# Optimization experiments

Measured on AMD Instinct MI355X. Metric: run time of the kernel, lower is better.

The kernel has to match this reference:

```python
import jax, jax.numpy as jnp
import numpy as np
from jax import lax


def _ln(x, gamma, beta, eps=1e-5):
    m = jnp.mean(x, -1, keepdims=True)
    v = jnp.mean(jnp.square(x - m), -1, keepdims=True)
    return (x - m) * lax.rsqrt(v + eps) * gamma + beta


def setup_inputs() -> dict:
    key = jax.random.key(0)
    ks = jax.random.split(key, 12)
    B, C, L = 16, 22, 3000
    D, D2, E, T, K = 64, 256, 8, 4, 13
    s = 0.02
    f32 = jnp.float32
    return dict(
        x_stream=jax.random.normal(ks[0], (B, C, L), f32),
        task_ids=jax.random.randint(ks[1], (B,), 0, T),
        conv_w=jax.random.normal(ks[2], (D, C, K), f32) * s,
        conv_b=jnp.zeros((D,), f32),
        cls_token=jax.random.normal(ks[3], (1, 1, D), f32) * s,
        tok_g=jnp.ones((D,), f32), tok_b=jnp.zeros((D,), f32),
        ds_conv_w=jax.random.normal(ks[4], (D2, 1, 1, K), f32) * s,
        ds_conv_b=jnp.zeros((D2,), f32),
        ds_comp_w=jax.random.normal(ks[5], (D2, D2, D), f32) * s,
        ds_comp_b=jnp.zeros((D2,), f32),
        ds_g=jnp.ones((D2,), f32), ds_b=jnp.zeros((D2,), f32),
        task_embed=jax.random.normal(ks[6], (T, D2), f32) * s,
        gate_w=jax.random.normal(ks[7], (2 * D2, E), f32) * s,
        gate_b=jnp.zeros((E,), f32),
        exp_w=jax.random.normal(ks[8], (E, D2, D2), f32) * s,
        exp_b=jnp.zeros((E, D2), f32),
        uni_w=jax.random.normal(ks[9], (D2, D2), f32) * s,
        uni_b=jnp.zeros((D2,), f32),
        out_g=jnp.ones((D2,), f32), out_b=jnp.zeros((D2,), f32),
    )


def reference(x_stream, task_ids, conv_w, conv_b, cls_token, tok_g, tok_b,
              ds_conv_w, ds_conv_b, ds_comp_w, ds_comp_b, ds_g, ds_b,
              task_embed, gate_w, gate_b, exp_w, exp_b, uni_w, uni_b,
              out_g, out_b):
    gelu = lambda x: jax.nn.gelu(x, approximate=False)
    # --- Tokenize1D: conv1d(stride 2, pad 6) -> GELU -> maxpool(3,3) -> cls cat -> LN
    h = lax.conv_general_dilated(x_stream, conv_w, (2,), [(6, 6)],
                                 dimension_numbers=('NCH', 'OIH', 'NCH')) + conv_b[:, None]
    h = gelu(h)
    h = lax.reduce_window(h, -jnp.inf, lax.max, (1, 1, 3), (1, 1, 3), 'VALID')
    h = jnp.transpose(h, (0, 2, 1))                       # [B, N0, D]
    B = h.shape[0]
    cls = jnp.broadcast_to(cls_token, (B, 1, cls_token.shape[-1]))
    h = jnp.concatenate([cls, h], axis=1)                 # [B, N, D]
    h = _ln(h, tok_g, tok_b)
    # --- DSConvBlock (depth 1): conv2d 1->D2 over (1,13), compress over dim, LN, GELU
    z = jnp.transpose(h, (0, 2, 1))[:, None]              # [B, 1, D, N]
    z = lax.conv_general_dilated(z, ds_conv_w, (1, 1), [(0, 0), (6, 6)],
                                 dimension_numbers=('NCHW', 'OIHW', 'NCHW'))
    z = z + ds_conv_b[:, None, None]                      # [B, D2, D, N]
    z = jnp.einsum('bcdn,ocd->bno', z, ds_comp_w) + ds_comp_b  # compress -> [B, N, D2]
    tokens = gelu(_ln(z, ds_g, ds_b))
    # --- TaskAwareMoE (eval: no dropout, no noise)
    Bn, N, D2 = tokens.shape
    t_vec = task_embed[task_ids]                          # [B, D2]
    T_cat = jnp.concatenate([tokens, jnp.broadcast_to(t_vec[:, None], (Bn, N, D2))], -1)
    logits = T_cat @ gate_w + gate_b                      # [B, N, E]
    topk_vals, topk_idx = lax.top_k(logits, 2)
    gates_k = jax.nn.softmax(topk_vals, axis=-1)          # softmax over top-k (rest are -inf -> 0)
    bi = jnp.arange(Bn)[:, None, None]
    ni = jnp.arange(N)[None, :, None]
    gates = jnp.zeros_like(logits).at[bi, ni, topk_idx].set(gates_k)
    expert_outs = gelu(jnp.einsum('bnd,edf->bnef', tokens, exp_w) + exp_b)  # [B,N,E,D2]
    T_task = jnp.einsum('bne,bnef->bnf', gates, expert_outs)
    T_univ = gelu(tokens @ uni_w + uni_b)
    omega = 1.0 - jnp.max(gates, axis=-1, keepdims=True)
    out = _ln(T_task + omega * T_univ, out_g, out_b)
    return out[:, 0, :]
```

## Files before the change

### kernel.cpp

```cpp
#include <hip/hip_runtime.h>
#include <hip/hip_bf16.h>
#include <math.h>

__device__ __forceinline__ float us2f(unsigned short u) {
    union { unsigned int i; float f; } cv;
    cv.i = ((unsigned int)u) << 16;
    return cv.f;
}

__device__ __forceinline__ int detect_bf(const void* ones_vec) {
    return ((const unsigned int*)ones_vec)[0] == 0x3F803F80u;
}

template<int BF>
__device__ __forceinline__ float ldg(const void* p, int i) {
    return BF ? us2f(((const unsigned short*)p)[i]) : ((const float*)p)[i];
}

__device__ __forceinline__ float wave_sum64(float v) {
#pragma unroll
    for (int m = 32; m > 0; m >>= 1) v += __shfl_xor(v, m, 64);
    return v;
}

__device__ __forceinline__ float gelu_exact(float x) {
    return 0.5f * x * (1.0f + erff(x * 0.7071067811865475f));
}

__device__ __forceinline__ float bsum16(float v, float* sh16) {
    int lane = threadIdx.x & 63, w = threadIdx.x >> 6;
    v = wave_sum64(v);
    __syncthreads();
    if (lane == 0) sh16[w] = v;
    __syncthreads();
    float s = 0;
#pragma unroll
    for (int i = 0; i < 16; ++i) s += sh16[i];
    return s;
}

#define SMEM1_BYTES 41216

template<int BF>
__device__ void stage1_m2(char* smem,
    const void* __restrict__ comp_w, const void* __restrict__ dconv_w,
    const void* __restrict__ dconv_b, const void* __restrict__ comp_b,
    float* __restrict__ M2, float* __restrict__ BE)
{
    int t = threadIdx.x, w = t >> 6, lane = t & 63;
    float* s_dsw = (float*)smem;
    float* s_dcb = s_dsw + 1792;
    float* sred  = s_dcb + 256;
    for (int i = t; i < 1792; i += 512) {
        int c = i / 7, j = i - c * 7;
        s_dsw[i] = ldg<BF>(dconv_w, c * 13 + 6 + j);
    }
    for (int i = t; i < 256; i += 512) s_dcb[i] = ldg<BF>(dconv_b, i);
    __syncthreads();

    int o = blockIdx.x;
    float a0 = 0, a1 = 0, a2 = 0, a3 = 0, a4 = 0, a5 = 0, a6 = 0, ab = 0;
    int base = o * 16384 + lane;
    int c0 = w * 32;
#pragma unroll 8
    for (int ci = 0; ci < 32; ++ci) {
        int c = c0 + ci;
        float wv = ldg<BF>(comp_w, base + c * 64);
        const float* ds = &s_dsw[c * 7];
        a0 += wv * ds[0]; a1 += wv * ds[1]; a2 += wv * ds[2]; a3 += wv * ds[3];
        a4 += wv * ds[4]; a5 += wv * ds[5]; a6 += wv * ds[6];
        ab += wv * s_dcb[c];
    }
    sred[(w * 8 + 0) * 64 + lane] = a0;
    sred[(w * 8 + 1) * 64 + lane] = a1;
    sred[(w * 8 + 2) * 64 + lane] = a2;
    sred[(w * 8 + 3) * 64 + lane] = a3;
    sred[(w * 8 + 4) * 64 + lane] = a4;
    sred[(w * 8 + 5) * 64 + lane] = a5;
    sred[(w * 8 + 6) * 64 + lane] = a6;
    sred[(w * 8 + 7) * 64 + lane] = ab;
    __syncthreads();
    if (t < 448) {
        int j = t >> 6, d = t & 63;
        float s = 0;
#pragma unroll
        for (int ww = 0; ww < 8; ++ww) s += sred[(ww * 8 + j) * 64 + d];
        M2[(j * 64 + d) * 256 + o] = s;
    } else {
        float s = 0;
#pragma unroll
        for (int ww = 0; ww < 8; ++ww) s += sred[(ww * 8 + 7) * 64 + lane];
        s = wave_sum64(s);
        if (lane == 0) BE[o] = ldg<BF>(comp_b, o) + s;
    }
}

template<int BF>
__device__ void stage1_tok(char* smem,
    const void* __restrict__ x, const void* __restrict__ conv_w,
    const void* __restrict__ conv_b, const void* __restrict__ cls,
    const void* __restrict__ tok_g, const void* __restrict__ tok_b,
    float* __restrict__ H)
{
    int t = threadIdx.x, b = blockIdx.x - 256;
    float* sx = (float*)smem;
    for (int i = t; i < 902; i += 512) {
        int c = i / 41, p = i - c * 41;
        sx[i] = ldg<BF>(x, (b * 22 + c) * 3000 + p);
    }
    int w = t >> 6, lane = t & 63, tt = w - 1;
    float val = 0.0f;
    if (BF) {
        unsigned short* swt = (unsigned short*)(smem + 3616);
        const unsigned short* cwu = (const unsigned short*)conv_w;
        for (int i = t; i < 64 * 286; i += 512) {
            int d = i / 286, r = i - d * 286;
            swt[r * 64 + d] = cwu[i];
        }
        __syncthreads();
        if (w == 0) val = ldg<BF>(cls, lane);
        else if (w <= 6) {
            float cb = ldg<BF>(conv_b, lane);
            float p0 = cb, p1 = cb, p2 = cb;
            for (int c = 0; c < 22; ++c) {
                const float* xr = &sx[c * 41];
#pragma unroll
                for (int k = 0; k < 13; ++k) {
                    float wv = us2f(swt[(c * 13 + k) * 64 + lane]);
                    int i0 = 6 * tt - 6 + k;
                    if (i0 >= 0)     p0 += xr[i0] * wv;
                    if (i0 + 2 >= 0) p1 += xr[i0 + 2] * wv;
                    if (i0 + 4 >= 0) p2 += xr[i0 + 4] * wv;
                }
            }
            val = fmaxf(fmaxf(gelu_exact(p0), gelu_exact(p1)), gelu_exact(p2));
        }
    } else {
        float* schunk = (float*)(smem + 3616);
        float cb = ldg<BF>(conv_b, lane);
        float p0 = cb, p1 = cb, p2 = cb;
        for (int c0 = 0; c0 < 22; c0 += 8) {
            int csz = (22 - c0 < 8) ? (22 - c0) : 8;
            int n = csz * 13 * 64;
            __syncthreads();
            for (int i = t; i < n; i += 512) {
                int d = i / (csz * 13), r = i - d * (csz * 13);
                schunk[r * 64 + d] = ldg<BF>(conv_w, d * 286 + c0 * 13 + r);
            }
            __syncthreads();
            if (w >= 1 && w <= 6) {
                for (int cc = 0; cc < csz; ++cc) {
                    const float* xr = &sx[(c0 + cc) * 41];
#pragma unroll
                    for (int k = 0; k < 13; ++k) {
                        float wv = schunk[(cc * 13 + k) * 64 + lane];
                        int i0 = 6 * tt - 6 + k;
                        if (i0 >= 0)     p0 += xr[i0] * wv;
                        if (i0 + 2 >= 0) p1 += xr[i0 + 2] * wv;
                        if (i0 + 4 >= 0) p2 += xr[i0 + 4] * wv;
                    }
                }
            }
        }
        val = (w == 0) ? ldg<BF>(cls, lane)
                       : fmaxf(fmaxf(gelu_exact(p0), gelu_exact(p1)), gelu_exact(p2));
    }
    if (w <= 6) {
        float mean = wave_sum64(val) * (1.0f / 64.0f);
        float dv = val - mean;
        float var = wave_sum64(dv * dv) * (1.0f / 64.0f);
        float hn = dv * rsqrtf(var + 1e-5f) * ldg<BF>(tok_g, lane) + ldg<BF>(tok_b, lane);
        H[b * 448 + w * 64 + lane] = hn;
    }
}

__global__ __launch_bounds__(512) void k_stage1(
    const void* __restrict__ x, const void* __restrict__ conv_w,
    const void* __restrict__ conv_b, const void* __restrict__ cls,
    const void* __restrict__ tok_g, const void* __restrict__ tok_b,
    const void* __restrict__ comp_w, const void* __restrict__ dconv_w,
    const void* __restrict__ dconv_b, const void* __restrict__ comp_b,
    float* __restrict__ H, float* __restrict__ M2, float* __restrict__ BE)
{
    __shared__ char smem[SMEM1_BYTES];
    int bf = detect_bf(tok_g);
    if (blockIdx.x < 256) {
        if (bf) stage1_m2<1>(smem, comp_w, dconv_w, dconv_b, comp_b, M2, BE);
        else    stage1_m2<0>(smem, comp_w, dconv_w, dconv_b, comp_b, M2, BE);
    } else {
        if (bf) stage1_tok<1>(smem, x, conv_w, conv_b, cls, tok_g, tok_b, H);
        else    stage1_tok<0>(smem, x, conv_w, conv_b, cls, tok_g, tok_b, H);
    }
}

template<int BF>
__device__ void stage2_body(char* smem,
    const float* __restrict__ H, const float* __restrict__ M2,
    const float* __restrict__ BE, const int* __restrict__ task_ids,
    const void* __restrict__ ds_g, const void* __restrict__ ds_b,
    const void* __restrict__ task_embed,
    const void* __restrict__ gate_w, const void* __restrict__ gate_b,
    const void* __restrict__ exp_w, const void* __restrict__ exp_b,
    const void* __restrict__ uni_w, const void* __restrict__ uni_b,
    const void* __restrict__ out_g, const void* __restrict__ out_b,
    void* __restrict__ out)
{
    float* sh_h   = (float*)smem;
    float* shp0   = sh_h + 448;
    float* shp1   = shp0 + 1024;
    float* shp2   = shp1 + 1024;
    float* sh_tok = shp2 + 1024;
    float* sh16   = sh_tok + 256;
    float* sh_g32 = sh16 + 16;
    float* sh_sc  = sh_g32 + 32;
    int*   sh_e   = (int*)(sh_sc + 4);

    int t = threadIdx.x, b = blockIdx.x;
    int o = t & 255, q = t >> 8, lane = t & 63, w = t >> 6;

    for (int i = t; i < 448; i += 1024) sh_h[i] = H[b * 448 + i];
    __syncthreads();

    float p = 0;
    int jd0 = q * 112;
#pragma unroll 8
    for (int j = 0; j < 112; ++j) {
        int jd = jd0 + j;
        p += M2[jd * 256 + o] * sh_h[jd];
    }
    shp0[q * 256 + o] = p;
    __syncthreads();

    float z = 0, dz = 0, tok = 0;
    if (t < 256)
        z = BE[o] + ((shp0[o] + shp0[256 + o]) + (shp0[512 + o] + shp0[768 + o]));
    float mean = bsum16((t < 256) ? z : 0.0f, sh16) * (1.0f / 256.0f);
    dz = z - mean;
    float var = bsum16((t < 256) ? dz * dz : 0.0f, sh16) * (1.0f / 256.0f);
    if (t < 256) {
        tok = gelu_exact(dz * rsqrtf(var + 1e-5f) * ldg<BF>(ds_g, o) + ldg<BF>(ds_b, o));
        sh_tok[o] = tok;
    }
    __syncthreads();

    int task = task_ids[b];
    {
        float tko = sh_tok[o];
        float tvo = ldg<BF>(task_embed, task * 256 + o);
        int ea = q * 2, eb = q * 2 + 1;
        float p0 = tko * ldg<BF>(gate_w, o * 8 + ea) + tvo * ldg<BF>(gate_w, (256 + o) * 8 + ea);
        float p1 = tko * ldg<BF>(gate_w, o * 8 + eb) + tvo * ldg<BF>(gate_w, (256 + o) * 8 + eb);
        p0 = wave_sum64(p0);
        p1 = wave_sum64(p1);
        if (lane == 0) { sh_g32[w * 2] = p0; sh_g32[w * 2 + 1] = p1; }
    }
    __syncthreads();
    if (t == 0) {
        float lg[8];
#pragma unroll
        for (int e = 0; e < 8; ++e) {
            int qq = e >> 1, r = e & 1;
            float s = ldg<BF>(gate_b, e);
#pragma unroll
            for (int i = 0; i < 4; ++i) s += sh_g32[(qq * 4 + i) * 2 + r];
            lg[e] = s;
        }
        int e0 = 0;
        for (int e = 1; e < 8; ++e) if (lg[e] > lg[e0]) e0 = e;
        int e1 = (e0 == 0) ? 1 : 0;
        for (int e = 0; e < 8; ++e) if (e != e0 && lg[e] > lg[e1]) e1 = e;
        float g0 = 1.0f / (1.0f + expf(lg[e1] - lg[e0]));
        sh_sc[0] = g0; sh_sc[1] = 1.0f - g0; sh_sc[2] = 1.0f - g0;
        sh_e[0] = e0; sh_e[1] = e1;
    }
    __syncthreads();
    int e0 = sh_e[0], e1 = sh_e[1];
    float g0 = sh_sc[0], g1 = sh_sc[1], om = sh_sc[2];

    float a0 = 0, a1 = 0, au = 0;
    int d0 = q * 64;
    int b0 = e0 * 65536 + o, b1 = e1 * 65536 + o;
#pragma unroll 8
    for (int i = 0; i < 64; ++i) {
        int d = d0 + i;
        float tk = sh_tok[d];
        a0 += tk * ldg<BF>(exp_w, b0 + d * 256);
        a1 += tk * ldg<BF>(exp_w, b1 + d * 256);
        au += tk * ldg<BF>(uni_w, o + d * 256);
    }
    shp0[q * 256 + o] = a0;
    shp1[q * 256 + o] = a1;
    shp2[q * 256 + o] = au;
    __syncthreads();

    float y = 0;
    if (t < 256) {
        float s0 = ldg<BF>(exp_b, e0 * 256 + o) + ((shp0[o] + shp0[256 + o]) + (shp0[512 + o] + shp0[768 + o]));
        float s1 = ldg<BF>(exp_b, e1 * 256 + o) + ((shp1[o] + shp1[256 + o]) + (shp1[512 + o] + shp1[768 + o]));
        float su = ldg<BF>(uni_b, o)            + ((shp2[o] + shp2[256 + o]) + (shp2[512 + o] + shp2[768 + o]));
        y = g0 * gelu_exact(s0) + g1 * gelu_exact(s1) + om * gelu_exact(su);
    }
    float m2v = bsum16((t < 256) ? y : 0.0f, sh16) * (1.0f / 256.0f);
    float dy = y - m2v;
    float v2 = bsum16((t < 256) ? dy * dy : 0.0f, sh16) * (1.0f / 256.0f);
    if (t < 256) {
        float res = dy * rsqrtf(v2 + 1e-5f) * ldg<BF>(out_g, o) + ldg<BF>(out_b, o);
        if (BF) ((__hip_bfloat16*)out)[b * 256 + o] = __float2bfloat16(res);
        else    ((float*)out)[b * 256 + o] = res;
    }
}

__global__ __launch_bounds__(1024) void k_stage2(
    const float* __restrict__ H, const float* __restrict__ M2,
    const float* __restrict__ BE, const int* __restrict__ task_ids,
    const void* __restrict__ tok_g,
    const void* __restrict__ ds_g, const void* __restrict__ ds_b,
    const void* __restrict__ task_embed,
    const void* __restrict__ gate_w, const void* __restrict__ gate_b,
    const void* __restrict__ exp_w, const void* __restrict__ exp_b,
    const void* __restrict__ uni_w, const void* __restrict__ uni_b,
    const void* __restrict__ out_g, const void* __restrict__ out_b,
    void* __restrict__ out)
{
    __shared__ char smem[(448 + 3 * 1024 + 256 + 16 + 32 + 4 + 2) * 4 + 16];
    int bf = detect_bf(tok_g);
    if (bf) stage2_body<1>(smem, H, M2, BE, task_ids, ds_g, ds_b, task_embed,
                           gate_w, gate_b, exp_w, exp_b, uni_w, uni_b,
                           out_g, out_b, out);
    else    stage2_body<0>(smem, H, M2, BE, task_ids, ds_g, ds_b, task_embed,
                           gate_w, gate_b, exp_w, exp_b, uni_w, uni_b,
                           out_g, out_b, out);
}

extern "C" void kernel_launch(void* const* d_in, const int* in_sizes, int n_in,
                              void* d_out, int out_size, void* d_ws, size_t ws_size,
                              hipStream_t stream) {
    const void* x         = d_in[0];
    const int* task_ids   = (const int*)d_in[1];
    const void* conv_w    = d_in[2];
    const void* conv_b    = d_in[3];
    const void* cls       = d_in[4];
    const void* tok_g     = d_in[5];
    const void* tok_b     = d_in[6];
    const void* ds_conv_w = d_in[7];
    const void* ds_conv_b = d_in[8];
    const void* ds_comp_w = d_in[9];
    const void* ds_comp_b = d_in[10];
    const void* ds_g      = d_in[11];
    const void* ds_b      = d_in[12];
    const void* task_embed= d_in[13];
    const void* gate_w    = d_in[14];
    const void* gate_b    = d_in[15];
    const void* exp_w     = d_in[16];
    const void* exp_b     = d_in[17];
    const void* uni_w     = d_in[18];
    const void* uni_b     = d_in[19];
    const void* out_g     = d_in[20];
    const void* out_b     = d_in[21];

    float* ws = (float*)d_ws;
    float* H  = ws;
    float* M2 = ws + 7168;
    float* BE = ws + 7168 + 114688;

    hipLaunchKernelGGL(k_stage1, dim3(272), dim3(512), 0, stream,
                       x, conv_w, conv_b, cls, tok_g, tok_b,
                       ds_comp_w, ds_conv_w, ds_conv_b, ds_comp_b,
                       H, M2, BE);
    hipLaunchKernelGGL(k_stage2, dim3(16), dim3(1024), 0, stream,
                       H, M2, BE, task_ids, tok_g, ds_g, ds_b, task_embed,
                       gate_w, gate_b, exp_w, exp_b, uni_w, uni_b,
                       out_g, out_b, d_out);
}
```

Measured before the change: 165.7 us.

## Halve M2 blocks, pad conv input and pre-transpose conv weights into shared memory

The stage-1 grid drops from 272 to 144 blocks: each M2 block now computes two output channels, and the tokenizer blocks start at index 128. The tokenizer zero-pads the input window in shared memory so the boundary branches go away. It stages all conv weights transposed with padding of 65 (bf16 weights packed in pairs), and loads x into registers with float2 reads. Several loops are unrolled 16 instead of 8. Shared memory per block grows to 80000 bytes, which may limit occupancy and add transpose cost.

```diff
diff --git a/kernel.cpp b/kernel.cpp
--- a/kernel.cpp
+++ b/kernel.cpp
@@ -39,7 +39,7 @@
     return s;
 }
 
-#define SMEM1_BYTES 41216
+#define SMEM1_BYTES 80000
 
 template<int BF>
 __device__ void stage1_m2(char* smem,
@@ -58,40 +58,43 @@
     for (int i = t; i < 256; i += 512) s_dcb[i] = ldg<BF>(dconv_b, i);
     __syncthreads();
 
-    int o = blockIdx.x;
-    float a0 = 0, a1 = 0, a2 = 0, a3 = 0, a4 = 0, a5 = 0, a6 = 0, ab = 0;
-    int base = o * 16384 + lane;
-    int c0 = w * 32;
-#pragma unroll 8
-    for (int ci = 0; ci < 32; ++ci) {
-        int c = c0 + ci;
-        float wv = ldg<BF>(comp_w, base + c * 64);
-        const float* ds = &s_dsw[c * 7];
-        a0 += wv * ds[0]; a1 += wv * ds[1]; a2 += wv * ds[2]; a3 += wv * ds[3];
-        a4 += wv * ds[4]; a5 += wv * ds[5]; a6 += wv * ds[6];
-        ab += wv * s_dcb[c];
-    }
-    sred[(w * 8 + 0) * 64 + lane] = a0;
-    sred[(w * 8 + 1) * 64 + lane] = a1;
-    sred[(w * 8 + 2) * 64 + lane] = a2;
-    sred[(w * 8 + 3) * 64 + lane] = a3;
-    sred[(w * 8 + 4) * 64 + lane] = a4;
-    sred[(w * 8 + 5) * 64 + lane] = a5;
-    sred[(w * 8 + 6) * 64 + lane] = a6;
-    sred[(w * 8 + 7) * 64 + lane] = ab;
-    __syncthreads();
-    if (t < 448) {
-        int j = t >> 6, d = t & 63;
-        float s = 0;
-#pragma unroll
-        for (int ww = 0; ww < 8; ++ww) s += sred[(ww * 8 + j) * 64 + d];
-        M2[(j * 64 + d) * 256 + o] = s;
-    } else {
-        float s = 0;
-#pragma unroll
-        for (int ww = 0; ww < 8; ++ww) s += sred[(ww * 8 + 7) * 64 + lane];
-        s = wave_sum64(s);
-        if (lane == 0) BE[o] = ldg<BF>(comp_b, o) + s;
+    for (int rep = 0; rep < 2; ++rep) {
+        int o = blockIdx.x + rep * 128;
+        float a0 = 0, a1 = 0, a2 = 0, a3 = 0, a4 = 0, a5 = 0, a6 = 0, ab = 0;
+        int base = o * 16384 + lane;
+        int c0 = w * 32;
+#pragma unroll 16
+        for (int ci = 0; ci < 32; ++ci) {
+            int c = c0 + ci;
+            float wv = ldg<BF>(comp_w, base + c * 64);
+            const float* ds = &s_dsw[c * 7];
+            a0 += wv * ds[0]; a1 += wv * ds[1]; a2 += wv * ds[2]; a3 += wv * ds[3];
+            a4 += wv * ds[4]; a5 += wv * ds[5]; a6 += wv * ds[6];
+            ab += wv * s_dcb[c];
+        }
+        if (rep) __syncthreads();
+        sred[(w * 8 + 0) * 64 + lane] = a0;
+        sred[(w * 8 + 1) * 64 + lane] = a1;
+        sred[(w * 8 + 2) * 64 + lane] = a2;
+        sred[(w * 8 + 3) * 64 + lane] = a3;
+        sred[(w * 8 + 4) * 64 + lane] = a4;
+        sred[(w * 8 + 5) * 64 + lane] = a5;
+        sred[(w * 8 + 6) * 64 + lane] = a6;
+        sred[(w * 8 + 7) * 64 + lane] = ab;
+        __syncthreads();
+        if (t < 448) {
+            int j = t >> 6, d = t & 63;
+            float s = 0;
+#pragma unroll
+            for (int ww = 0; ww < 8; ++ww) s += sred[(ww * 8 + j) * 64 + d];
+            M2[(j * 64 + d) * 256 + o] = s;
+        } else {
+            float s = 0;
+#pragma unroll
+            for (int ww = 0; ww < 8; ++ww) s += sred[(ww * 8 + 7) * 64 + lane];
+            s = wave_sum64(s);
+            if (lane == 0) BE[o] = ldg<BF>(comp_b, o) + s;
+        }
     }
 }
 
@@ -102,69 +105,89 @@
     const void* __restrict__ tok_g, const void* __restrict__ tok_b,
     float* __restrict__ H)
 {
-    int t = threadIdx.x, b = blockIdx.x - 256;
-    float* sx = (float*)smem;
-    for (int i = t; i < 902; i += 512) {
-        int c = i / 41, p = i - c * 41;
-        sx[i] = ldg<BF>(x, (b * 22 + c) * 3000 + p);
+    int t = threadIdx.x, b = blockIdx.x - 128;
+    float* sxp = (float*)smem;
+    for (int i = t; i < 22 * 64; i += 512) {
+        int c = i >> 6, j = i & 63;
+        float v = 0.0f;
+        if (j >= 6 && j < 47) v = ldg<BF>(x, (b * 22 + c) * 3000 + (j - 6));
+        sxp[i] = v;
     }
     int w = t >> 6, lane = t & 63, tt = w - 1;
     float val = 0.0f;
+
     if (BF) {
-        unsigned short* swt = (unsigned short*)(smem + 3616);
+        unsigned int* sw2 = (unsigned int*)(smem + 5632);
         const unsigned short* cwu = (const unsigned short*)conv_w;
-        for (int i = t; i < 64 * 286; i += 512) {
-            int d = i / 286, r = i - d * 286;
-            swt[r * 64 + d] = cwu[i];
+        for (int i = t; i < 154 * 64; i += 512) {
+            int d = i / 154, ck2 = i - d * 154;
+            int c = ck2 / 7, kp = ck2 - c * 7;
+            unsigned int lo = cwu[d * 286 + c * 13 + 2 * kp];
+            unsigned int hi = (kp < 6) ? cwu[d * 286 + c * 13 + 2 * kp + 1] : 0u;
+            sw2[ck2 * 65 + d] = lo | (hi << 16);
         }
         __syncthreads();
-        if (w == 0) val = ldg<BF>(cls, lane);
-        else if (w <= 6) {
+        if (w >= 1 && w <= 6) {
             float cb = ldg<BF>(conv_b, lane);
             float p0 = cb, p1 = cb, p2 = cb;
             for (int c = 0; c < 22; ++c) {
-                const float* xr = &sx[c * 41];
-#pragma unroll
-                for (int k = 0; k < 13; ++k) {
-                    float wv = us2f(swt[(c * 13 + k) * 64 + lane]);
-                    int i0 = 6 * tt - 6 + k;
-                    if (i0 >= 0)     p0 += xr[i0] * wv;
-                    if (i0 + 2 >= 0) p1 += xr[i0 + 2] * wv;
-                    if (i0 + 4 >= 0) p2 += xr[i0 + 4] * wv;
+                float xv[18];
+                const float* xr = &sxp[c * 64 + 6 * tt];
+#pragma unroll
+                for (int i = 0; i < 8; ++i) {
+                    float2 q = *(const float2*)&xr[2 * i];
+                    xv[2 * i] = q.x; xv[2 * i + 1] = q.y;
+                }
+                xv[16] = xr[16];
+                xv[17] = 0.0f;
+                const unsigned int* wr = &sw2[c * 7 * 65 + lane];
+#pragma unroll
+                for (int kp = 0; kp < 7; ++kp) {
+                    unsigned int pr = wr[kp * 65];
+                    float w0 = us2f((unsigned short)(pr & 0xffff));
+                    float w1 = us2f((unsigned short)(pr >> 16));
+                    p0 += xv[2 * kp]     * w0 + xv[2 * kp + 1] * w1;
+                    p1 += xv[2 * kp + 2] * w0 + xv[2 * kp + 3] * w1;
+                    p2 += xv[2 * kp + 4] * w0 + xv[2 * kp + 5] * w1;
                 }
             }
             val = fmaxf(fmaxf(gelu_exact(p0), gelu_exact(p1)), gelu_exact(p2));
+        } else if (w == 0) {
+            val = ldg<BF>(cls, lane);
         }
     } else {
-        float* schunk = (float*)(smem + 3616);
-        float cb = ldg<BF>(conv_b, lane);
-        float p0 = cb, p1 = cb, p2 = cb;
-        for (int c0 = 0; c0 < 22; c0 += 8) {
-            int csz = (22 - c0 < 8) ? (22 - c0) : 8;
-            int n = csz * 13 * 64;
-            __syncthreads();
-            for (int i = t; i < n; i += 512) {
-                int d = i / (csz * 13), r = i - d * (csz * 13);
-                schunk[r * 64 + d] = ldg<BF>(conv_w, d * 286 + c0 * 13 + r);
-            }
-            __syncthreads();
-            if (w >= 1 && w <= 6) {
-                for (int cc = 0; cc < csz; ++cc) {
-                    const float* xr = &sx[(c0 + cc) * 41];
-#pragma unroll
-                    for (int k = 0; k < 13; ++k) {
-                        float wv = schunk[(cc * 13 + k) * 64 + lane];
-                        int i0 = 6 * tt - 6 + k;
-                        if (i0 >= 0)     p0 += xr[i0] * wv;
-                        if (i0 + 2 >= 0) p1 += xr[i0 + 2] * wv;
-                        if (i0 + 4 >= 0) p2 += xr[i0 + 4] * wv;
-                    }
+        float* sfw = (float*)(smem + 5632);
+        const float* cwf = (const float*)conv_w;
+        for (int i = t; i < 286 * 64; i += 512) {
+            int d = i / 286, ck = i - d * 286;
+            sfw[ck * 65 + d] = cwf[d * 286 + ck];
+        }
+        __syncthreads();
+        if (w >= 1 && w <= 6) {
+            float cb = ldg<BF>(conv_b, lane);
+            float p0 = cb, p1 = cb, p2 = cb;
+            for (int c = 0; c < 22; ++c) {
+                float xv[17];
+                const float* xr = &sxp[c * 64 + 6 * tt];
+#pragma unroll
+                for (int i = 0; i < 8; ++i) {
+                    float2 q = *(const float2*)&xr[2 * i];
+                    xv[2 * i] = q.x; xv[2 * i + 1] = q.y;
+                }
+                xv[16] = xr[16];
+                const float* wr = &sfw[c * 13 * 65 + lane];
+#pragma unroll
+                for (int k = 0; k < 13; ++k) {
+                    float wv = wr[k * 65];
+                    p0 += xv[k] * wv; p1 += xv[k + 2] * wv; p2 += xv[k + 4] * wv;
                 }
             }
-        }
-        val = (w == 0) ? ldg<BF>(cls, lane)
-                       : fmaxf(fmaxf(gelu_exact(p0), gelu_exact(p1)), gelu_exact(p2));
-    }
+            val = fmaxf(fmaxf(gelu_exact(p0), gelu_exact(p1)), gelu_exact(p2));
+        } else if (w == 0) {
+            val = ldg<BF>(cls, lane);
+        }
+    }
+
     if (w <= 6) {
         float mean = wave_sum64(val) * (1.0f / 64.0f);
         float dv = val - mean;
@@ -184,7 +207,7 @@
 {
     __shared__ char smem[SMEM1_BYTES];
     int bf = detect_bf(tok_g);
-    if (blockIdx.x < 256) {
+    if (blockIdx.x < 128) {
         if (bf) stage1_m2<1>(smem, comp_w, dconv_w, dconv_b, comp_b, M2, BE);
         else    stage1_m2<0>(smem, comp_w, dconv_w, dconv_b, comp_b, M2, BE);
     } else {
@@ -223,7 +246,7 @@
 
     float p = 0;
     int jd0 = q * 112;
-#pragma unroll 8
+#pragma unroll 16
     for (int j = 0; j < 112; ++j) {
         int jd = jd0 + j;
         p += M2[jd * 256 + o] * sh_h[jd];
@@ -280,7 +303,7 @@
     float a0 = 0, a1 = 0, au = 0;
     int d0 = q * 64;
     int b0 = e0 * 65536 + o, b1 = e1 * 65536 + o;
-#pragma unroll 8
+#pragma unroll 16
     for (int i = 0; i < 64; ++i) {
         int d = d0 + i;
         float tk = sh_tok[d];
@@ -363,7 +386,7 @@
     float* M2 = ws + 7168;
     float* BE = ws + 7168 + 114688;
 
-    hipLaunchKernelGGL(k_stage1, dim3(272), dim3(512), 0, stream,
+    hipLaunchKernelGGL(k_stage1, dim3(144), dim3(512), 0, stream,
                        x, conv_w, conv_b, cls, tok_g, tok_b,
                        ds_comp_w, ds_conv_w, ds_conv_b, ds_comp_b,
                        H, M2, BE);
```

After: 211.2 us. +27.5%, slower.
